# Performance work log

Hardware: AMD Instinct MI355X
Metric: run time of the kernel (lower is better)

## Reference

```python
import jax, jax.numpy as jnp
import numpy as np

N = 500000
D = 128
R = D // 4  # reduction = 4
G = 2048    # number of graphs


def setup_inputs() -> dict:
    key = jax.random.key(0)
    ks = jax.random.split(key, 8)
    x = jax.random.normal(ks[0], (N, D), dtype=jnp.float32)
    batch = jnp.sort(jax.random.randint(ks[1], (N,), 0, G))
    # SE-gate MLP params (nn.Linear stores weight as [out,in]; we store transposed for x @ W)
    fc_w1 = jax.random.normal(ks[2], (D, R), dtype=jnp.float32) * (1.0 / np.sqrt(D))
    fc_b1 = jnp.zeros((R,), dtype=jnp.float32)
    fc_w2 = jax.random.normal(ks[3], (R, D), dtype=jnp.float32) * (1.0 / np.sqrt(R))
    fc_b2 = jnp.zeros((D,), dtype=jnp.float32)
    # xavier-uniform weight_matrix [D, D]
    lim = np.sqrt(6.0 / (D + D))
    W = jax.random.uniform(ks[4], (D, D), dtype=jnp.float32, minval=-lim, maxval=lim)
    return {"x": x, "batch": batch, "size": G,
            "fc_w1": fc_w1, "fc_b1": fc_b1, "fc_w2": fc_w2, "fc_b2": fc_b2, "W": W}


def reference(x, batch, size, fc_w1, fc_b1, fc_w2, fc_b2, W):
    # gated SE-block: attention = tanh(MLP(x)); x = attention*x + x
    attention = jnp.tanh(jnp.maximum(x @ fc_w1 + fc_b1, 0.0) @ fc_w2 + fc_b2)
    x2 = attention * x + x  # [N, D]
    # global_mean_pool: segment mean over graphs
    seg_sum = jax.ops.segment_sum(x2, batch, num_segments=size)           # [G, D]
    counts = jax.ops.segment_sum(jnp.ones((x2.shape[0],), x2.dtype), batch, num_segments=size)
    mean = seg_sum / jnp.maximum(counts, 1.0)[:, None]                     # [G, D]
    transformed_global = jnp.tanh(mean @ W)                                # [G, D]
    # gather-broadcast per-graph global back to nodes, per-node attention coef
    coefs = jax.nn.sigmoid(jnp.sum(x2 * transformed_global[batch], axis=1))  # [N]
    weighted = coefs[:, None] * x2                                          # [N, D]
    return jax.ops.segment_sum(weighted, batch, num_segments=size)          # [G, D]
```

## Files before the change

### kernel.cpp

```cpp
#include <hip/hip_runtime.h>
#include <hip/hip_bf16.h>

#define DDIM 128
#define RDIM 32
#define BLK  256
#define CAP  216
#define XS2  132
#define HSTR 40

typedef __attribute__((ext_vector_type(8))) short bf16x8;
typedef __attribute__((ext_vector_type(4))) float f32x4;

__device__ __forceinline__ float tanh_fast(float v) {
  float e = __expf(2.f * v);
  return 1.f - 2.f / (e + 1.f);
}
__device__ __forceinline__ float sigmoid_fast(float v) {
  return 1.f / (1.f + __expf(-v));
}
__device__ __forceinline__ unsigned short f2bf(float f) {
  unsigned u = __float_as_uint(f);
  u += 0x7fffu + ((u >> 16) & 1u);
  return (unsigned short)(u >> 16);
}
__device__ __forceinline__ float bf2f(unsigned short s) {
  return __uint_as_float(((unsigned)s) << 16);
}
__device__ __forceinline__ unsigned pkbf(float lo, float hi) {
  __hip_bfloat162 t2 = __float22bfloat162_rn(make_float2(lo, hi));
  return *reinterpret_cast<unsigned*>(&t2);
}
__device__ __forceinline__ int lower_bound(const int* __restrict__ b, int n, int v) {
  int lo = 0, hi = n;
  while (lo < hi) { int m = (lo + hi) >> 1; if (b[m] < v) lo = m + 1; else hi = m; }
  return lo;
}

__global__ void k0_prep(const float* __restrict__ w1, const float* __restrict__ w2,
                        unsigned short* __restrict__ w1tf, unsigned short* __restrict__ w2tf)
{
  const int i  = blockIdx.x * blockDim.x + threadIdx.x;
  const int l  = i & 63;
  const int lr = l & 15, q = l >> 4;
  if (i < 512) {
    const int frag = i >> 6;
    const int mt2 = frag >> 2, kk = frag & 3;
    bf16x8 v;
    #pragma unroll
    for (int j = 0; j < 8; ++j)
      v[j] = (short)f2bf(w1[(size_t)(kk * 32 + q * 8 + j) * RDIM + mt2 * 16 + lr]);
    *(bf16x8*)&w1tf[(size_t)i * 8] = v;
  } else {
    const int mt = (i - 512) >> 6;
    bf16x8 v;
    #pragma unroll
    for (int j = 0; j < 8; ++j)
      v[j] = (short)f2bf(w2[(size_t)(q * 8 + j) * DDIM + mt * 16 + lr]);
    *(bf16x8*)&w2tf[(size_t)(i - 512) * 8] = v;
  }
}

__global__ void kb_bounds(const int* __restrict__ batch, int* __restrict__ bounds,
                          int N, int G)
{
  const int g = blockIdx.x * blockDim.x + threadIdx.x;
  if (g <= G) bounds[g] = lower_bound(batch, N, g);
}

__global__ __launch_bounds__(BLK, 2) void k_fused(
    const float* __restrict__ x,
    const unsigned short* __restrict__ w1tf, const float* __restrict__ b1,
    const unsigned short* __restrict__ w2tf, const float* __restrict__ b2,
    const float* __restrict__ W, const int* __restrict__ bounds,
    float* __restrict__ out, int N)
{
  __shared__ unsigned short x2s[CAP * XS2];
  __shared__ unsigned short hs4[4][16 * HSTR];
  __shared__ float part[4][132];
  __shared__ float meanv[DDIM];
  __shared__ float tgs[DDIM];

  const int t  = threadIdx.x;
  const int l  = t & 63;
  const int wv = t >> 6;
  const int lr = l & 15;
  const int q  = l >> 4;
  const int g  = blockIdx.x;
  const int lo = bounds[g], hi = bounds[g + 1];
  const int cnt = hi - lo;
  unsigned short* hs = hs4[wv];

  bf16x8 w1r[2][4], w2r[8];
  #pragma unroll
  for (int mt2 = 0; mt2 < 2; ++mt2)
    #pragma unroll
    for (int kk = 0; kk < 4; ++kk)
      w1r[mt2][kk] = *(const bf16x8*)&w1tf[(size_t)((mt2 * 4 + kk) * 64 + l) * 8];
  #pragma unroll
  for (int mt = 0; mt < 8; ++mt)
    w2r[mt] = *(const bf16x8*)&w2tf[(size_t)(mt * 64 + l) * 8];

  auto mlp16 = [&](int tb, float (&y)[8][4]) {
    const int ridx = tb + lr;
    const int rcl  = (ridx < cnt) ? ridx : (cnt > 0 ? cnt - 1 : 0);
    const float* xrow = x + (size_t)(lo + rcl) * DDIM;
    bf16x8 xf[4];
    #pragma unroll
    for (int kk = 0; kk < 4; ++kk) {
      float4 a = *(const float4*)(xrow + kk * 32 + q * 8);
      float4 b = *(const float4*)(xrow + kk * 32 + q * 8 + 4);
      uint4 u;
      u.x = pkbf(a.x, a.y); u.y = pkbf(a.z, a.w);
      u.z = pkbf(b.x, b.y); u.w = pkbf(b.z, b.w);
      xf[kk] = *(bf16x8*)&u;
    }
    f32x4 hacc[2];
    {
      float4 bv0 = *(const float4*)(b1 + q * 4);
      float4 bv1 = *(const float4*)(b1 + 16 + q * 4);
      hacc[0][0] = bv0.x; hacc[0][1] = bv0.y; hacc[0][2] = bv0.z; hacc[0][3] = bv0.w;
      hacc[1][0] = bv1.x; hacc[1][1] = bv1.y; hacc[1][2] = bv1.z; hacc[1][3] = bv1.w;
    }
    #pragma unroll
    for (int kk = 0; kk < 4; ++kk) {
      hacc[0] = __builtin_amdgcn_mfma_f32_16x16x32_bf16(w1r[0][kk], xf[kk], hacc[0], 0, 0, 0);
      hacc[1] = __builtin_amdgcn_mfma_f32_16x16x32_bf16(w1r[1][kk], xf[kk], hacc[1], 0, 0, 0);
    }
    #pragma unroll
    for (int mt2 = 0; mt2 < 2; ++mt2) {
      float h0 = fmaxf(hacc[mt2][0], 0.f), h1 = fmaxf(hacc[mt2][1], 0.f);
      float h2 = fmaxf(hacc[mt2][2], 0.f), h3 = fmaxf(hacc[mt2][3], 0.f);
      uint2 p; p.x = pkbf(h0, h1); p.y = pkbf(h2, h3);
      *(uint2*)&hs[lr * HSTR + mt2 * 16 + q * 4] = p;
    }
    bf16x8 ah = *(const bf16x8*)&hs[lr * HSTR + q * 8];
    f32x4 cacc[8];
    #pragma unroll
    for (int mt = 0; mt < 8; ++mt)
      #pragma unroll
      for (int c = 0; c < 4; ++c) cacc[mt][c] = 0.f;
    #pragma unroll
    for (int mt = 0; mt < 8; ++mt)
      cacc[mt] = __builtin_amdgcn_mfma_f32_16x16x32_bf16(w2r[mt], ah, cacc[mt], 0, 0, 0);
    #pragma unroll
    for (int mt = 0; mt < 8; ++mt) {
      float4 xg = *(const float4*)(xrow + mt * 16 + q * 4);
      float4 bv = *(const float4*)(b2 + mt * 16 + q * 4);
      y[mt][0] = xg.x * (1.f + tanh_fast(cacc[mt][0] + bv.x));
      y[mt][1] = xg.y * (1.f + tanh_fast(cacc[mt][1] + bv.y));
      y[mt][2] = xg.z * (1.f + tanh_fast(cacc[mt][2] + bv.z));
      y[mt][3] = xg.w * (1.f + tanh_fast(cacc[mt][3] + bv.w));
    }
  };

  float macc[8][4];
  #pragma unroll
  for (int mt = 0; mt < 8; ++mt)
    #pragma unroll
    for (int c = 0; c < 4; ++c) macc[mt][c] = 0.f;

  for (int it = 0; it * 64 < cnt; ++it) {
    const int tb = it * 64 + wv * 16;
    if (tb >= cnt) continue;
    float y[8][4];
    mlp16(tb, y);
    const int ridx = tb + lr;
    if (ridx < cnt) {
      #pragma unroll
      for (int mt = 0; mt < 8; ++mt) {
        macc[mt][0] += y[mt][0]; macc[mt][1] += y[mt][1];
        macc[mt][2] += y[mt][2]; macc[mt][3] += y[mt][3];
        if (ridx < CAP) {
          uint2 p; p.x = pkbf(y[mt][0], y[mt][1]); p.y = pkbf(y[mt][2], y[mt][3]);
          *(uint2*)&x2s[ridx * XS2 + mt * 16 + q * 4] = p;
        }
      }
    }
  }
  __syncthreads();

  #pragma unroll
  for (int mt = 0; mt < 8; ++mt)
    #pragma unroll
    for (int c = 0; c < 4; ++c) {
      float v = macc[mt][c];
      v += __shfl_xor(v, 1, 64);
      v += __shfl_xor(v, 2, 64);
      v += __shfl_xor(v, 4, 64);
      v += __shfl_xor(v, 8, 64);
      macc[mt][c] = v;
    }
  if (lr == 0) {
    #pragma unroll
    for (int mt = 0; mt < 8; ++mt)
      *(float4*)&part[wv][mt * 16 + q * 4] =
          make_float4(macc[mt][0], macc[mt][1], macc[mt][2], macc[mt][3]);
  }
  __syncthreads();
  if (t < DDIM) {
    float m = part[0][t] + part[1][t] + part[2][t] + part[3][t];
    meanv[t] = (cnt > 0) ? m / (float)cnt : 0.f;
  }
  __syncthreads();
  if (t < DDIM) {
    float a = 0.f;
    #pragma unroll 8
    for (int k = 0; k < DDIM; ++k) a = fmaf(meanv[k], W[k * DDIM + t], a);
    tgs[t] = tanh_fast(a);
  }
  __syncthreads();

  float tgv[8][4];
  #pragma unroll
  for (int mt = 0; mt < 8; ++mt) {
    float4 tv = *(const float4*)&tgs[mt * 16 + q * 4];
    tgv[mt][0] = tv.x; tgv[mt][1] = tv.y; tgv[mt][2] = tv.z; tgv[mt][3] = tv.w;
  }
  float oacc[8][4];
  #pragma unroll
  for (int mt = 0; mt < 8; ++mt)
    #pragma unroll
    for (int c = 0; c < 4; ++c) oacc[mt][c] = 0.f;

  const int cap2 = cnt < CAP ? cnt : CAP;
  for (int it = 0; it * 64 < cap2; ++it) {
    const int tb = it * 64 + wv * 16;
    if (tb >= cap2) continue;
    const int ridx = tb + lr;
    const bool v = ridx < cap2;
    float xv[8][4];
    #pragma unroll
    for (int mt = 0; mt < 8; ++mt) {
      if (v) {
        uint2 u = *(const uint2*)&x2s[ridx * XS2 + mt * 16 + q * 4];
        xv[mt][0] = bf2f((unsigned short)(u.x & 0xffffu));
        xv[mt][1] = bf2f((unsigned short)(u.x >> 16));
        xv[mt][2] = bf2f((unsigned short)(u.y & 0xffffu));
        xv[mt][3] = bf2f((unsigned short)(u.y >> 16));
      } else {
        xv[mt][0] = xv[mt][1] = xv[mt][2] = xv[mt][3] = 0.f;
      }
    }
    float p = 0.f;
    #pragma unroll
    for (int mt = 0; mt < 8; ++mt)
      #pragma unroll
      for (int c = 0; c < 4; ++c) p = fmaf(xv[mt][c], tgv[mt][c], p);
    p += __shfl_xor(p, 16, 64);
    p += __shfl_xor(p, 32, 64);
    const float coef = sigmoid_fast(p);
    #pragma unroll
    for (int mt = 0; mt < 8; ++mt)
      #pragma unroll
      for (int c = 0; c < 4; ++c) oacc[mt][c] = fmaf(coef, xv[mt][c], oacc[mt][c]);
  }
  for (int it = 0; CAP + it * 64 < cnt; ++it) {
    const int tb = CAP + it * 64 + wv * 16;
    if (tb >= cnt) continue;
    float y[8][4];
    mlp16(tb, y);
    const int ridx = tb + lr;
    const bool v = ridx < cnt;
    float p = 0.f;
    if (v) {
      #pragma unroll
      for (int mt = 0; mt < 8; ++mt)
        #pragma unroll
        for (int c = 0; c < 4; ++c) p = fmaf(y[mt][c], tgv[mt][c], p);
    }
    p += __shfl_xor(p, 16, 64);
    p += __shfl_xor(p, 32, 64);
    const float coef = v ? sigmoid_fast(p) : 0.f;
    #pragma unroll
    for (int mt = 0; mt < 8; ++mt)
      #pragma unroll
      for (int c = 0; c < 4; ++c) oacc[mt][c] = fmaf(coef, v ? y[mt][c] : 0.f, oacc[mt][c]);
  }
  __syncthreads();

  #pragma unroll
  for (int mt = 0; mt < 8; ++mt)
    #pragma unroll
    for (int c = 0; c < 4; ++c) {
      float v = oacc[mt][c];
      v += __shfl_xor(v, 1, 64);
      v += __shfl_xor(v, 2, 64);
      v += __shfl_xor(v, 4, 64);
      v += __shfl_xor(v, 8, 64);
      oacc[mt][c] = v;
    }
  if (lr == 0) {
    #pragma unroll
    for (int mt = 0; mt < 8; ++mt)
      *(float4*)&part[wv][mt * 16 + q * 4] =
          make_float4(oacc[mt][0], oacc[mt][1], oacc[mt][2], oacc[mt][3]);
  }
  __syncthreads();
  if (t < DDIM)
    out[(size_t)g * DDIM + t] = part[0][t] + part[1][t] + part[2][t] + part[3][t];
}

extern "C" void kernel_launch(void* const* d_in, const int* in_sizes, int n_in,
                              void* d_out, int out_size, void* d_ws, size_t ws_size,
                              hipStream_t stream) {
  const float* x     = (const float*)d_in[0];
  const int*   batch = (const int*)d_in[1];
  const float* w1 = (const float*)d_in[3];
  const float* b1 = (const float*)d_in[4];
  const float* w2 = (const float*)d_in[5];
  const float* b2 = (const float*)d_in[6];
  const float* W  = (const float*)d_in[7];
  float* out = (float*)d_out;

  const int N = in_sizes[0] / DDIM;
  const int G = out_size / DDIM;

  unsigned short* w1tf = (unsigned short*)d_ws;
  unsigned short* w2tf = w1tf + 4096;
  int* bounds = (int*)(w2tf + 4096);
  (void)ws_size; (void)n_in;

  hipLaunchKernelGGL(k0_prep, dim3(4), dim3(BLK), 0, stream, w1, w2, w1tf, w2tf);
  hipLaunchKernelGGL(kb_bounds, dim3((G + 1 + BLK - 1) / BLK), dim3(BLK), 0, stream,
                     batch, bounds, N, G);
  hipLaunchKernelGGL(k_fused, dim3(G), dim3(BLK), 0, stream,
                     x, w1tf, b1, w2tf, b2, W, bounds, out, N);
}
```

Measured before the change: 145.1 us.

## Double fused block width, stage MLP weights in LDS, split W matvec across threads

The fused per-graph kernel grows from 4 to 8 waves (512 threads, launch bounds min 4 blocks) and now keeps the SE-MLP bf16 weights in shared memory instead of per-lane registers. This frees VGPRs for higher occupancy. The cached-row capacity CAP shrinks from 216 to 160 to fit LDS, so graphs larger than 160 nodes recompute more rows in the overflow pass. The mean@W matvec is split over 4 k-slices using all 512 threads, the b2 bias is folded into the MFMA accumulator init, and the overflow pass rounds x2 through bf16 to match the cached path.

```diff
diff --git a/kernel.cpp b/kernel.cpp
--- a/kernel.cpp
+++ b/kernel.cpp
@@ -3,9 +3,10 @@
 
 #define DDIM 128
 #define RDIM 32
-#define BLK  256
-#define CAP  216
-#define XS2  132
+#define PBLK 256
+#define BLK  512
+#define CAP  160
+#define XS2  136
 #define HSTR 40
 
 typedef __attribute__((ext_vector_type(8))) short bf16x8;
@@ -67,42 +68,40 @@
   if (g <= G) bounds[g] = lower_bound(batch, N, g);
 }
 
-__global__ __launch_bounds__(BLK, 2) void k_fused(
+__global__ __launch_bounds__(BLK, 4) void k_fused(
     const float* __restrict__ x,
     const unsigned short* __restrict__ w1tf, const float* __restrict__ b1,
     const unsigned short* __restrict__ w2tf, const float* __restrict__ b2,
     const float* __restrict__ W, const int* __restrict__ bounds,
     float* __restrict__ out, int N)
 {
+  __shared__ unsigned short w1t[512 * 8];
+  __shared__ unsigned short w2t[512 * 8];
   __shared__ unsigned short x2s[CAP * XS2];
-  __shared__ unsigned short hs4[4][16 * HSTR];
-  __shared__ float part[4][132];
+  __shared__ unsigned short hs8[8][16 * HSTR];
+  __shared__ float part[8][132];
   __shared__ float meanv[DDIM];
   __shared__ float tgs[DDIM];
 
   const int t  = threadIdx.x;
   const int l  = t & 63;
-  const int wv = t >> 6;
+  const int w  = t >> 6;
   const int lr = l & 15;
   const int q  = l >> 4;
   const int g  = blockIdx.x;
   const int lo = bounds[g], hi = bounds[g + 1];
   const int cnt = hi - lo;
-  unsigned short* hs = hs4[wv];
-
-  bf16x8 w1r[2][4], w2r[8];
-  #pragma unroll
-  for (int mt2 = 0; mt2 < 2; ++mt2)
-    #pragma unroll
-    for (int kk = 0; kk < 4; ++kk)
-      w1r[mt2][kk] = *(const bf16x8*)&w1tf[(size_t)((mt2 * 4 + kk) * 64 + l) * 8];
-  #pragma unroll
-  for (int mt = 0; mt < 8; ++mt)
-    w2r[mt] = *(const bf16x8*)&w2tf[(size_t)(mt * 64 + l) * 8];
-
-  auto mlp16 = [&](int tb, float (&y)[8][4]) {
+  unsigned short* hs = hs8[w];
+
+  for (int i = t; i < 512; i += BLK) {
+    ((bf16x8*)w1t)[i] = ((const bf16x8*)w1tf)[i];
+    ((bf16x8*)w2t)[i] = ((const bf16x8*)w2tf)[i];
+  }
+  __syncthreads();
+
+  auto core = [&](int tb, f32x4 (&cacc)[8]) -> const float* {
     const int ridx = tb + lr;
-    const int rcl  = (ridx < cnt) ? ridx : (cnt > 0 ? cnt - 1 : 0);
+    const int rcl  = min(ridx, cnt - 1);
     const float* xrow = x + (size_t)(lo + rcl) * DDIM;
     bf16x8 xf[4];
     #pragma unroll
@@ -123,8 +122,10 @@
     }
     #pragma unroll
     for (int kk = 0; kk < 4; ++kk) {
-      hacc[0] = __builtin_amdgcn_mfma_f32_16x16x32_bf16(w1r[0][kk], xf[kk], hacc[0], 0, 0, 0);
-      hacc[1] = __builtin_amdgcn_mfma_f32_16x16x32_bf16(w1r[1][kk], xf[kk], hacc[1], 0, 0, 0);
+      bf16x8 wa = *(const bf16x8*)&w1t[(size_t)((0 * 4 + kk) * 64 + l) * 8];
+      bf16x8 wb = *(const bf16x8*)&w1t[(size_t)((1 * 4 + kk) * 64 + l) * 8];
+      hacc[0] = __builtin_amdgcn_mfma_f32_16x16x32_bf16(wa, xf[kk], hacc[0], 0, 0, 0);
+      hacc[1] = __builtin_amdgcn_mfma_f32_16x16x32_bf16(wb, xf[kk], hacc[1], 0, 0, 0);
     }
     #pragma unroll
     for (int mt2 = 0; mt2 < 2; ++mt2) {
@@ -134,23 +135,17 @@
       *(uint2*)&hs[lr * HSTR + mt2 * 16 + q * 4] = p;
     }
     bf16x8 ah = *(const bf16x8*)&hs[lr * HSTR + q * 8];
-    f32x4 cacc[8];
-    #pragma unroll
-    for (int mt = 0; mt < 8; ++mt)
-      #pragma unroll
-      for (int c = 0; c < 4; ++c) cacc[mt][c] = 0.f;
-    #pragma unroll
-    for (int mt = 0; mt < 8; ++mt)
-      cacc[mt] = __builtin_amdgcn_mfma_f32_16x16x32_bf16(w2r[mt], ah, cacc[mt], 0, 0, 0);
     #pragma unroll
     for (int mt = 0; mt < 8; ++mt) {
-      float4 xg = *(const float4*)(xrow + mt * 16 + q * 4);
       float4 bv = *(const float4*)(b2 + mt * 16 + q * 4);
-      y[mt][0] = xg.x * (1.f + tanh_fast(cacc[mt][0] + bv.x));
-      y[mt][1] = xg.y * (1.f + tanh_fast(cacc[mt][1] + bv.y));
-      y[mt][2] = xg.z * (1.f + tanh_fast(cacc[mt][2] + bv.z));
-      y[mt][3] = xg.w * (1.f + tanh_fast(cacc[mt][3] + bv.w));
-    }
+      cacc[mt][0] = bv.x; cacc[mt][1] = bv.y; cacc[mt][2] = bv.z; cacc[mt][3] = bv.w;
+    }
+    #pragma unroll
+    for (int mt = 0; mt < 8; ++mt) {
+      bf16x8 wf = *(const bf16x8*)&w2t[(size_t)(mt * 64 + l) * 8];
+      cacc[mt] = __builtin_amdgcn_mfma_f32_16x16x32_bf16(wf, ah, cacc[mt], 0, 0, 0);
+    }
+    return xrow;
   };
 
   float macc[8][4];
@@ -159,19 +154,25 @@
     #pragma unroll
     for (int c = 0; c < 4; ++c) macc[mt][c] = 0.f;
 
-  for (int it = 0; it * 64 < cnt; ++it) {
-    const int tb = it * 64 + wv * 16;
+  const int niter1 = (cnt + 127) >> 7;
+  for (int it = 0; it < niter1; ++it) {
+    const int tb = it * 128 + w * 16;
     if (tb >= cnt) continue;
-    float y[8][4];
-    mlp16(tb, y);
+    f32x4 cacc[8];
+    const float* xrow = core(tb, cacc);
     const int ridx = tb + lr;
     if (ridx < cnt) {
       #pragma unroll
       for (int mt = 0; mt < 8; ++mt) {
-        macc[mt][0] += y[mt][0]; macc[mt][1] += y[mt][1];
-        macc[mt][2] += y[mt][2]; macc[mt][3] += y[mt][3];
+        float4 xg = *(const float4*)(xrow + mt * 16 + q * 4);
+        float y0 = xg.x * (1.f + tanh_fast(cacc[mt][0]));
+        float y1 = xg.y * (1.f + tanh_fast(cacc[mt][1]));
+        float y2 = xg.z * (1.f + tanh_fast(cacc[mt][2]));
+        float y3 = xg.w * (1.f + tanh_fast(cacc[mt][3]));
+        macc[mt][0] += y0; macc[mt][1] += y1;
+        macc[mt][2] += y2; macc[mt][3] += y3;
         if (ridx < CAP) {
-          uint2 p; p.x = pkbf(y[mt][0], y[mt][1]); p.y = pkbf(y[mt][2], y[mt][3]);
+          uint2 p; p.x = pkbf(y0, y1); p.y = pkbf(y2, y3);
           *(uint2*)&x2s[ridx * XS2 + mt * 16 + q * 4] = p;
         }
       }
@@ -193,29 +194,31 @@
   if (lr == 0) {
     #pragma unroll
     for (int mt = 0; mt < 8; ++mt)
-      *(float4*)&part[wv][mt * 16 + q * 4] =
+      *(float4*)&part[w][mt * 16 + q * 4] =
           make_float4(macc[mt][0], macc[mt][1], macc[mt][2], macc[mt][3]);
   }
   __syncthreads();
   if (t < DDIM) {
-    float m = part[0][t] + part[1][t] + part[2][t] + part[3][t];
+    float m = 0.f;
+    #pragma unroll
+    for (int w2 = 0; w2 < 8; ++w2) m += part[w2][t];
     meanv[t] = (cnt > 0) ? m / (float)cnt : 0.f;
   }
   __syncthreads();
-  if (t < DDIM) {
+
+  {
+    const int c = t & 127, s = t >> 7;
     float a = 0.f;
-    #pragma unroll 8
-    for (int k = 0; k < DDIM; ++k) a = fmaf(meanv[k], W[k * DDIM + t], a);
-    tgs[t] = tanh_fast(a);
-  }
-  __syncthreads();
-
-  float tgv[8][4];
-  #pragma unroll
-  for (int mt = 0; mt < 8; ++mt) {
-    float4 tv = *(const float4*)&tgs[mt * 16 + q * 4];
-    tgv[mt][0] = tv.x; tgv[mt][1] = tv.y; tgv[mt][2] = tv.z; tgv[mt][3] = tv.w;
-  }
+    #pragma unroll
+    for (int k = 0; k < 32; ++k)
+      a = fmaf(meanv[s * 32 + k], W[(size_t)(s * 32 + k) * DDIM + c], a);
+    part[s][c] = a;
+  }
+  __syncthreads();
+  if (t < DDIM)
+    tgs[t] = tanh_fast(part[0][t] + part[1][t] + part[2][t] + part[3][t]);
+  __syncthreads();
+
   float oacc[8][4];
   #pragma unroll
   for (int mt = 0; mt < 8; ++mt)
@@ -223,58 +226,73 @@
     for (int c = 0; c < 4; ++c) oacc[mt][c] = 0.f;
 
   const int cap2 = cnt < CAP ? cnt : CAP;
-  for (int it = 0; it * 64 < cap2; ++it) {
-    const int tb = it * 64 + wv * 16;
+  const int niter2 = (cap2 + 127) >> 7;
+  for (int it = 0; it < niter2; ++it) {
+    const int tb = it * 128 + w * 16;
     if (tb >= cap2) continue;
     const int ridx = tb + lr;
     const bool v = ridx < cap2;
+    const int rr = v ? ridx : 0;
     float xv[8][4];
+    float p = 0.f;
     #pragma unroll
     for (int mt = 0; mt < 8; ++mt) {
-      if (v) {
-        uint2 u = *(const uint2*)&x2s[ridx * XS2 + mt * 16 + q * 4];
-        xv[mt][0] = bf2f((unsigned short)(u.x & 0xffffu));
-        xv[mt][1] = bf2f((unsigned short)(u.x >> 16));
-        xv[mt][2] = bf2f((unsigned short)(u.y & 0xffffu));
-        xv[mt][3] = bf2f((unsigned short)(u.y >> 16));
-      } else {
-        xv[mt][0] = xv[mt][1] = xv[mt][2] = xv[mt][3] = 0.f;
-      }
-    }
-    float p = 0.f;
-    #pragma unroll
-    for (int mt = 0; mt < 8; ++mt)
-      #pragma unroll
-      for (int c = 0; c < 4; ++c) p = fmaf(xv[mt][c], tgv[mt][c], p);
+      uint2 u = *(const uint2*)&x2s[rr * XS2 + mt * 16 + q * 4];
+      xv[mt][0] = bf2f((unsigned short)(u.x & 0xffffu));
+      xv[mt][1] = bf2f((unsigned short)(u.x >> 16));
+      xv[mt][2] = bf2f((unsigned short)(u.y & 0xffffu));
+      xv[mt][3] = bf2f((unsigned short)(u.y >> 16));
+      float4 tg4 = *(const float4*)&tgs[mt * 16 + q * 4];
+      p = fmaf(xv[mt][0], tg4.x, p); p = fmaf(xv[mt][1], tg4.y, p);
+      p = fmaf(xv[mt][2], tg4.z, p); p = fmaf(xv[mt][3], tg4.w, p);
+    }
     p += __shfl_xor(p, 16, 64);
     p += __shfl_xor(p, 32, 64);
     const float coef = sigmoid_fast(p);
-    #pragma unroll
-    for (int mt = 0; mt < 8; ++mt)
-      #pragma unroll
-      for (int c = 0; c < 4; ++c) oacc[mt][c] = fmaf(coef, xv[mt][c], oacc[mt][c]);
-  }
-  for (int it = 0; CAP + it * 64 < cnt; ++it) {
-    const int tb = CAP + it * 64 + wv * 16;
-    if (tb >= cnt) continue;
-    float y[8][4];
-    mlp16(tb, y);
-    const int ridx = tb + lr;
-    const bool v = ridx < cnt;
-    float p = 0.f;
     if (v) {
       #pragma unroll
       for (int mt = 0; mt < 8; ++mt)
         #pragma unroll
-        for (int c = 0; c < 4; ++c) p = fmaf(y[mt][c], tgv[mt][c], p);
-    }
-    p += __shfl_xor(p, 16, 64);
-    p += __shfl_xor(p, 32, 64);
-    const float coef = v ? sigmoid_fast(p) : 0.f;
-    #pragma unroll
-    for (int mt = 0; mt < 8; ++mt)
+        for (int c = 0; c < 4; ++c) oacc[mt][c] = fmaf(coef, xv[mt][c], oacc[mt][c]);
+    }
+  }
+
+  if (cnt > CAP) {
+    const int niter3 = (cnt - CAP + 127) >> 7;
+    for (int it = 0; it < niter3; ++it) {
+      const int tb = CAP + it * 128 + w * 16;
+      if (tb >= cnt) continue;
+      f32x4 cacc[8];
+      const float* xrow = core(tb, cacc);
+      const int ridx = tb + lr;
+      const bool v = ridx < cnt;
+      float p = 0.f;
+      uint2 y2[8];
       #pragma unroll
-      for (int c = 0; c < 4; ++c) oacc[mt][c] = fmaf(coef, v ? y[mt][c] : 0.f, oacc[mt][c]);
+      for (int mt = 0; mt < 8; ++mt) {
+        float4 xg = *(const float4*)(xrow + mt * 16 + q * 4);
+        float y0 = xg.x * (1.f + tanh_fast(cacc[mt][0]));
+        float y1 = xg.y * (1.f + tanh_fast(cacc[mt][1]));
+        float y2v = xg.z * (1.f + tanh_fast(cacc[mt][2]));
+        float y3 = xg.w * (1.f + tanh_fast(cacc[mt][3]));
+        float4 tg4 = *(const float4*)&tgs[mt * 16 + q * 4];
+        p = fmaf(y0, tg4.x, p); p = fmaf(y1, tg4.y, p);
+        p = fmaf(y2v, tg4.z, p); p = fmaf(y3, tg4.w, p);
+        y2[mt].x = pkbf(y0, y1); y2[mt].y = pkbf(y2v, y3);
+      }
+      p += __shfl_xor(p, 16, 64);
+      p += __shfl_xor(p, 32, 64);
+      const float coef = sigmoid_fast(p);
+      if (v) {
+        #pragma unroll
+        for (int mt = 0; mt < 8; ++mt) {
+          oacc[mt][0] = fmaf(coef, bf2f((unsigned short)(y2[mt].x & 0xffffu)), oacc[mt][0]);
+          oacc[mt][1] = fmaf(coef, bf2f((unsigned short)(y2[mt].x >> 16)),     oacc[mt][1]);
+          oacc[mt][2] = fmaf(coef, bf2f((unsigned short)(y2[mt].y & 0xffffu)), oacc[mt][2]);
+          oacc[mt][3] = fmaf(coef, bf2f((unsigned short)(y2[mt].y >> 16)),     oacc[mt][3]);
+        }
+      }
+    }
   }
   __syncthreads();
 
@@ -292,12 +310,16 @@
   if (lr == 0) {
     #pragma unroll
     for (int mt = 0; mt < 8; ++mt)
-      *(float4*)&part[wv][mt * 16 + q * 4] =
+      *(float4*)&part[w][mt * 16 + q * 4] =
           make_float4(oacc[mt][0], oacc[mt][1], oacc[mt][2], oacc[mt][3]);
   }
   __syncthreads();
-  if (t < DDIM)
-    out[(size_t)g * DDIM + t] = part[0][t] + part[1][t] + part[2][t] + part[3][t];
+  if (t < DDIM) {
+    float m = 0.f;
+    #pragma unroll
+    for (int w2 = 0; w2 < 8; ++w2) m += part[w2][t];
+    out[(size_t)g * DDIM + t] = m;
+  }
 }
 
 extern "C" void kernel_launch(void* const* d_in, const int* in_sizes, int n_in,
@@ -320,8 +342,8 @@
   int* bounds = (int*)(w2tf + 4096);
   (void)ws_size; (void)n_in;
 
-  hipLaunchKernelGGL(k0_prep, dim3(4), dim3(BLK), 0, stream, w1, w2, w1tf, w2tf);
-  hipLaunchKernelGGL(kb_bounds, dim3((G + 1 + BLK - 1) / BLK), dim3(BLK), 0, stream,
+  hipLaunchKernelGGL(k0_prep, dim3(4), dim3(PBLK), 0, stream, w1, w2, w1tf, w2tf);
+  hipLaunchKernelGGL(kb_bounds, dim3((G + 1 + PBLK - 1) / PBLK), dim3(PBLK), 0, stream,
                      batch, bounds, N, G);
   hipLaunchKernelGGL(k_fused, dim3(G), dim3(BLK), 0, stream,
                      x, w1tf, b1, w2tf, b2, W, bounds, out, N);
```

Result: slower. 156.5 us (+7.8%).

## Stream x tiles through double-buffered LDS ring and recompute MLP in second pass

Applied to the files above, without the earlier changes.

Drops the bf16 LDS cache of x2, so both passes recompute the SE-gate MLP. Each pass streams 16-row x tiles per wave into a swizzled, double-buffered LDS ring using global_load_lds async copies, with vmcnt waits so the next tile loads while the current one is computed. Also folds the b2 bias into the MFMA accumulator init, uses hardware rcp in tanh/sigmoid, splits the mean@W matvec across all 256 threads, and exits early on empty graphs. The aim is to hide global latency and improve load coalescing, at the cost of doubling MLP compute and reading x twice for every graph instead of only the large ones.

```diff
diff --git a/kernel.cpp b/kernel.cpp
--- a/kernel.cpp
+++ b/kernel.cpp
@@ -3,9 +3,8 @@
 
 #define DDIM 128
 #define RDIM 32
+#define PBLK 256
 #define BLK  256
-#define CAP  216
-#define XS2  132
 #define HSTR 40
 
 typedef __attribute__((ext_vector_type(8))) short bf16x8;
@@ -13,10 +12,10 @@
 
 __device__ __forceinline__ float tanh_fast(float v) {
   float e = __expf(2.f * v);
-  return 1.f - 2.f / (e + 1.f);
+  return 1.f - 2.f * __builtin_amdgcn_rcpf(e + 1.f);
 }
 __device__ __forceinline__ float sigmoid_fast(float v) {
-  return 1.f / (1.f + __expf(-v));
+  return __builtin_amdgcn_rcpf(1.f + __expf(-v));
 }
 __device__ __forceinline__ unsigned short f2bf(float f) {
   unsigned u = __float_as_uint(f);
@@ -74,7 +73,7 @@
     const float* __restrict__ W, const int* __restrict__ bounds,
     float* __restrict__ out, int N)
 {
-  __shared__ unsigned short x2s[CAP * XS2];
+  __shared__ float ring[4][2][2048];
   __shared__ unsigned short hs4[4][16 * HSTR];
   __shared__ float part[4][132];
   __shared__ float meanv[DDIM];
@@ -82,13 +81,15 @@
 
   const int t  = threadIdx.x;
   const int l  = t & 63;
-  const int wv = t >> 6;
+  const int w  = t >> 6;
   const int lr = l & 15;
   const int q  = l >> 4;
   const int g  = blockIdx.x;
   const int lo = bounds[g], hi = bounds[g + 1];
   const int cnt = hi - lo;
-  unsigned short* hs = hs4[wv];
+  unsigned short* hs = hs4[w];
+
+  if (cnt <= 0) { if (t < DDIM) out[(size_t)g * DDIM + t] = 0.f; return; }
 
   bf16x8 w1r[2][4], w2r[8];
   #pragma unroll
@@ -100,15 +101,31 @@
   for (int mt = 0; mt < 8; ++mt)
     w2r[mt] = *(const bf16x8*)&w2tf[(size_t)(mt * 64 + l) * 8];
 
-  auto mlp16 = [&](int tb, float (&y)[8][4]) {
-    const int ridx = tb + lr;
-    const int rcl  = (ridx < cnt) ? ridx : (cnt > 0 ? cnt - 1 : 0);
-    const float* xrow = x + (size_t)(lo + rcl) * DDIM;
+  const int sr  = l >> 5;
+  const int sc  = l & 31;
+  const int swz = lr & 7;
+  const int ntile = (cnt + 15) >> 4;
+
+  auto fill = [&](int s, int tb) {
+    float* lds = ring[w][s];
+    #pragma unroll
+    for (int j = 0; j < 8; ++j) {
+      const int r   = j * 2 + sr;
+      const int row = lo + min(tb + r, cnt - 1);
+      const int lc  = sc ^ (r & 7);
+      __builtin_amdgcn_global_load_lds(x + (size_t)row * DDIM + lc * 4,
+                                       lds + j * 256, 16, 0, 0);
+    }
+  };
+
+  auto mlp = [&](int s, float (&y)[8][4]) {
+    float* lds = ring[w][s];
     bf16x8 xf[4];
     #pragma unroll
     for (int kk = 0; kk < 4; ++kk) {
-      float4 a = *(const float4*)(xrow + kk * 32 + q * 8);
-      float4 b = *(const float4*)(xrow + kk * 32 + q * 8 + 4);
+      const int c0 = kk * 8 + q * 2;
+      float4 a = *(const float4*)&lds[lr * 128 + ((c0    ) ^ swz) * 4];
+      float4 b = *(const float4*)&lds[lr * 128 + ((c0 + 1) ^ swz) * 4];
       uint4 u;
       u.x = pkbf(a.x, a.y); u.y = pkbf(a.z, a.w);
       u.z = pkbf(b.x, b.y); u.w = pkbf(b.z, b.w);
@@ -136,20 +153,20 @@
     bf16x8 ah = *(const bf16x8*)&hs[lr * HSTR + q * 8];
     f32x4 cacc[8];
     #pragma unroll
-    for (int mt = 0; mt < 8; ++mt)
-      #pragma unroll
-      for (int c = 0; c < 4; ++c) cacc[mt][c] = 0.f;
+    for (int mt = 0; mt < 8; ++mt) {
+      float4 bv = *(const float4*)(b2 + mt * 16 + q * 4);
+      cacc[mt][0] = bv.x; cacc[mt][1] = bv.y; cacc[mt][2] = bv.z; cacc[mt][3] = bv.w;
+    }
     #pragma unroll
     for (int mt = 0; mt < 8; ++mt)
       cacc[mt] = __builtin_amdgcn_mfma_f32_16x16x32_bf16(w2r[mt], ah, cacc[mt], 0, 0, 0);
     #pragma unroll
     for (int mt = 0; mt < 8; ++mt) {
-      float4 xg = *(const float4*)(xrow + mt * 16 + q * 4);
-      float4 bv = *(const float4*)(b2 + mt * 16 + q * 4);
-      y[mt][0] = xg.x * (1.f + tanh_fast(cacc[mt][0] + bv.x));
-      y[mt][1] = xg.y * (1.f + tanh_fast(cacc[mt][1] + bv.y));
-      y[mt][2] = xg.z * (1.f + tanh_fast(cacc[mt][2] + bv.z));
-      y[mt][3] = xg.w * (1.f + tanh_fast(cacc[mt][3] + bv.w));
+      float4 xg = *(const float4*)&lds[lr * 128 + ((mt * 4 + q) ^ swz) * 4];
+      y[mt][0] = xg.x * (1.f + tanh_fast(cacc[mt][0]));
+      y[mt][1] = xg.y * (1.f + tanh_fast(cacc[mt][1]));
+      y[mt][2] = xg.z * (1.f + tanh_fast(cacc[mt][2]));
+      y[mt][3] = xg.w * (1.f + tanh_fast(cacc[mt][3]));
     }
   };
 
@@ -159,22 +176,26 @@
     #pragma unroll
     for (int c = 0; c < 4; ++c) macc[mt][c] = 0.f;
 
-  for (int it = 0; it * 64 < cnt; ++it) {
-    const int tb = it * 64 + wv * 16;
-    if (tb >= cnt) continue;
-    float y[8][4];
-    mlp16(tb, y);
-    const int ridx = tb + lr;
-    if (ridx < cnt) {
-      #pragma unroll
-      for (int mt = 0; mt < 8; ++mt) {
-        macc[mt][0] += y[mt][0]; macc[mt][1] += y[mt][1];
-        macc[mt][2] += y[mt][2]; macc[mt][3] += y[mt][3];
-        if (ridx < CAP) {
-          uint2 p; p.x = pkbf(y[mt][0], y[mt][1]); p.y = pkbf(y[mt][2], y[mt][3]);
-          *(uint2*)&x2s[ridx * XS2 + mt * 16 + q * 4] = p;
-        }
-      }
+  {
+    int ti = w, cur = 0;
+    if (ti < ntile) fill(cur, ti * 16);
+    for (; ti < ntile; ti += 4) {
+      const int tn = ti + 4;
+      if (tn < ntile) {
+        fill(cur ^ 1, tn * 16);
+        asm volatile("s_waitcnt vmcnt(8)" ::: "memory");
+      } else {
+        asm volatile("s_waitcnt vmcnt(0)" ::: "memory");
+      }
+      float y[8][4];
+      mlp(cur, y);
+      if (ti * 16 + lr < cnt) {
+        #pragma unroll
+        for (int mt = 0; mt < 8; ++mt)
+          #pragma unroll
+          for (int c = 0; c < 4; ++c) macc[mt][c] += y[mt][c];
+      }
+      cur ^= 1;
     }
   }
   __syncthreads();
@@ -193,88 +214,66 @@
   if (lr == 0) {
     #pragma unroll
     for (int mt = 0; mt < 8; ++mt)
-      *(float4*)&part[wv][mt * 16 + q * 4] =
+      *(float4*)&part[w][mt * 16 + q * 4] =
           make_float4(macc[mt][0], macc[mt][1], macc[mt][2], macc[mt][3]);
   }
   __syncthreads();
   if (t < DDIM) {
     float m = part[0][t] + part[1][t] + part[2][t] + part[3][t];
-    meanv[t] = (cnt > 0) ? m / (float)cnt : 0.f;
-  }
-  __syncthreads();
-  if (t < DDIM) {
+    meanv[t] = m / (float)cnt;
+  }
+  __syncthreads();
+
+  {
+    const int c = t & 127, s = t >> 7;
     float a = 0.f;
     #pragma unroll 8
-    for (int k = 0; k < DDIM; ++k) a = fmaf(meanv[k], W[k * DDIM + t], a);
-    tgs[t] = tanh_fast(a);
-  }
-  __syncthreads();
-
-  float tgv[8][4];
-  #pragma unroll
-  for (int mt = 0; mt < 8; ++mt) {
-    float4 tv = *(const float4*)&tgs[mt * 16 + q * 4];
-    tgv[mt][0] = tv.x; tgv[mt][1] = tv.y; tgv[mt][2] = tv.z; tgv[mt][3] = tv.w;
-  }
+    for (int k = 0; k < 64; ++k)
+      a = fmaf(meanv[s * 64 + k], W[(size_t)(s * 64 + k) * DDIM + c], a);
+    part[s][c] = a;
+  }
+  __syncthreads();
+  if (t < DDIM) tgs[t] = tanh_fast(part[0][t] + part[1][t]);
+  __syncthreads();
+
   float oacc[8][4];
   #pragma unroll
   for (int mt = 0; mt < 8; ++mt)
     #pragma unroll
     for (int c = 0; c < 4; ++c) oacc[mt][c] = 0.f;
 
-  const int cap2 = cnt < CAP ? cnt : CAP;
-  for (int it = 0; it * 64 < cap2; ++it) {
-    const int tb = it * 64 + wv * 16;
-    if (tb >= cap2) continue;
-    const int ridx = tb + lr;
-    const bool v = ridx < cap2;
-    float xv[8][4];
-    #pragma unroll
-    for (int mt = 0; mt < 8; ++mt) {
-      if (v) {
-        uint2 u = *(const uint2*)&x2s[ridx * XS2 + mt * 16 + q * 4];
-        xv[mt][0] = bf2f((unsigned short)(u.x & 0xffffu));
-        xv[mt][1] = bf2f((unsigned short)(u.x >> 16));
-        xv[mt][2] = bf2f((unsigned short)(u.y & 0xffffu));
-        xv[mt][3] = bf2f((unsigned short)(u.y >> 16));
+  {
+    int ti = w, cur = 0;
+    if (ti < ntile) fill(cur, ti * 16);
+    for (; ti < ntile; ti += 4) {
+      const int tn = ti + 4;
+      if (tn < ntile) {
+        fill(cur ^ 1, tn * 16);
+        asm volatile("s_waitcnt vmcnt(8)" ::: "memory");
       } else {
-        xv[mt][0] = xv[mt][1] = xv[mt][2] = xv[mt][3] = 0.f;
-      }
-    }
-    float p = 0.f;
-    #pragma unroll
-    for (int mt = 0; mt < 8; ++mt)
+        asm volatile("s_waitcnt vmcnt(0)" ::: "memory");
+      }
+      float y[8][4];
+      mlp(cur, y);
+      float p = 0.f;
       #pragma unroll
-      for (int c = 0; c < 4; ++c) p = fmaf(xv[mt][c], tgv[mt][c], p);
-    p += __shfl_xor(p, 16, 64);
-    p += __shfl_xor(p, 32, 64);
-    const float coef = sigmoid_fast(p);
-    #pragma unroll
-    for (int mt = 0; mt < 8; ++mt)
-      #pragma unroll
-      for (int c = 0; c < 4; ++c) oacc[mt][c] = fmaf(coef, xv[mt][c], oacc[mt][c]);
-  }
-  for (int it = 0; CAP + it * 64 < cnt; ++it) {
-    const int tb = CAP + it * 64 + wv * 16;
-    if (tb >= cnt) continue;
-    float y[8][4];
-    mlp16(tb, y);
-    const int ridx = tb + lr;
-    const bool v = ridx < cnt;
-    float p = 0.f;
-    if (v) {
-      #pragma unroll
-      for (int mt = 0; mt < 8; ++mt)
+      for (int mt = 0; mt < 8; ++mt) {
+        float4 tg4 = *(const float4*)&tgs[mt * 16 + q * 4];
+        p = fmaf(y[mt][0], tg4.x, p); p = fmaf(y[mt][1], tg4.y, p);
+        p = fmaf(y[mt][2], tg4.z, p); p = fmaf(y[mt][3], tg4.w, p);
+      }
+      p += __shfl_xor(p, 16, 64);
+      p += __shfl_xor(p, 32, 64);
+      const float coef = sigmoid_fast(p);
+      if (ti * 16 + lr < cnt) {
         #pragma unroll
-        for (int c = 0; c < 4; ++c) p = fmaf(y[mt][c], tgv[mt][c], p);
-    }
-    p += __shfl_xor(p, 16, 64);
-    p += __shfl_xor(p, 32, 64);
-    const float coef = v ? sigmoid_fast(p) : 0.f;
-    #pragma unroll
-    for (int mt = 0; mt < 8; ++mt)
-      #pragma unroll
-      for (int c = 0; c < 4; ++c) oacc[mt][c] = fmaf(coef, v ? y[mt][c] : 0.f, oacc[mt][c]);
+        for (int mt = 0; mt < 8; ++mt)
+          #pragma unroll
+          for (int c = 0; c < 4; ++c)
+            oacc[mt][c] = fmaf(coef, y[mt][c], oacc[mt][c]);
+      }
+      cur ^= 1;
+    }
   }
   __syncthreads();
 
@@ -292,7 +291,7 @@
   if (lr == 0) {
     #pragma unroll
     for (int mt = 0; mt < 8; ++mt)
-      *(float4*)&part[wv][mt * 16 + q * 4] =
+      *(float4*)&part[w][mt * 16 + q * 4] =
           make_float4(oacc[mt][0], oacc[mt][1], oacc[mt][2], oacc[mt][3]);
   }
   __syncthreads();
@@ -320,8 +319,8 @@
   int* bounds = (int*)(w2tf + 4096);
   (void)ws_size; (void)n_in;
 
-  hipLaunchKernelGGL(k0_prep, dim3(4), dim3(BLK), 0, stream, w1, w2, w1tf, w2tf);
-  hipLaunchKernelGGL(kb_bounds, dim3((G + 1 + BLK - 1) / BLK), dim3(BLK), 0, stream,
+  hipLaunchKernelGGL(k0_prep, dim3(4), dim3(PBLK), 0, stream, w1, w2, w1tf, w2tf);
+  hipLaunchKernelGGL(kb_bounds, dim3((G + 1 + PBLK - 1) / PBLK), dim3(PBLK), 0, stream,
                      batch, bounds, N, G);
   hipLaunchKernelGGL(k_fused, dim3(G), dim3(BLK), 0, stream,
                      x, w1tf, b1, w2tf, b2, W, bounds, out, N);
```

New measurement: 134.3 us. 1.08x faster.
